# Kernel optimization log

Hardware: AMD Instinct MI355X
Metric: run time of the kernel (lower is better)

## Reference

```python
import jax, jax.numpy as jnp
import numpy as np
import math

BLUR_K = [1.0, 3.0, 3.0, 1.0]
EPS = 1e-8


def _make_blur_kernel(upsample_factor=2):
    k = jnp.asarray(BLUR_K, dtype=jnp.float32)
    k = k[None, :] * k[:, None]
    k = k / k.sum()
    return k * (upsample_factor ** 2)


def setup_inputs() -> dict:
    key = jax.random.key(0)
    ks = jax.random.split(key, 5)
    B, Cin, Cout, K, S, H, W = 16, 256, 128, 3, 512, 64, 64
    x = jax.random.normal(ks[0], (B, Cin, H, W), dtype=jnp.float32)
    style = jax.random.normal(ks[1], (B, S), dtype=jnp.float32)
    weight = jax.random.normal(ks[2], (1, Cout, Cin, K, K), dtype=jnp.float32)
    mod_w = jax.random.normal(ks[3], (Cin, S), dtype=jnp.float32) * (1.0 / math.sqrt(S))
    mod_b = jnp.ones((Cin,), dtype=jnp.float32)  # StyleGAN2 modulation bias init = 1
    return {"x": x, "style": style, "weight": weight, "mod_w": mod_w, "mod_b": mod_b}


def reference(x, style, weight, mod_w, mod_b):
    B, Cin, H, W = x.shape
    Cout = weight.shape[1]
    K = weight.shape[-1]
    scale = 1.0 / math.sqrt(Cin * K * K)

    # modulation: Linear(style_dim -> in_channel)
    s = style @ mod_w.T + mod_b                      # (B, Cin)
    w = scale * weight * s[:, None, :, None, None]   # (B, Cout, Cin, K, K)
    demod = jax.lax.rsqrt(jnp.sum(w * w, axis=(2, 3, 4)) + EPS)  # (B, Cout)
    w = w * demod[:, :, None, None, None]

    # per-sample conv_transpose2d(stride=2, padding=0, groups=B)
    # == lhs-dilated grouped correlation with spatially-flipped kernel
    kernel = jnp.flip(w, axis=(3, 4)).reshape(B * Cout, Cin, K, K)
    xg = x.reshape(1, B * Cin, H, W)
    out = jax.lax.conv_general_dilated(
        xg, kernel,
        window_strides=(1, 1),
        padding=((K - 1, K - 1), (K - 1, K - 1)),
        lhs_dilation=(2, 2),
        feature_group_count=B,
        dimension_numbers=("NCHW", "OIHW", "NCHW"),
    )  # (1, B*Cout, 2H+K-2, 2W+K-2) -> here (1, B*Cout, 2H+1, 2W+1)
    Ht, Wt = out.shape[2], out.shape[3]

    # Blur2 / upfirdn2d(up=1, down=1, pad=(pad0, pad1))
    # p = len(blur_kernel) - 2 - (K - 1); pad0 = (p+1)//2 + 1; pad1 = p//2 + 1
    p = len(BLUR_K) - 2 - (K - 1)
    pad0 = (p + 1) // 2 + 1
    pad1 = p // 2 + 1
    bk = _make_blur_kernel()                       # (4, 4)
    bw = jnp.flip(bk, axis=(0, 1))[None, None]     # (1, 1, 4, 4)
    outs = out.reshape(B * Cout, 1, Ht, Wt)
    blurred = jax.lax.conv_general_dilated(
        outs, bw,
        window_strides=(1, 1),
        padding=((pad0, pad1), (pad0, pad1)),
        dimension_numbers=("NCHW", "OIHW", "NCHW"),
    )
    Hb, Wb = blurred.shape[2], blurred.shape[3]
    return blurred.reshape(B, Cout, Hb, Wb)
```

## Files before the change

kernel.cpp:

```cpp
#include <hip/hip_runtime.h>
#include <stdint.h>

#define CIN 256
#define COUT 128
#define SDIM 512
#define NB 16

#define XP_RSTRIDE 16896
#define XP_BSTRIDE 1115136
#define A_BSTRIDE (512*2304)

typedef __attribute__((ext_vector_type(8))) short short8;
typedef __attribute__((ext_vector_type(4))) float f32x4;

__device__ __forceinline__ float bf2f(unsigned short h) {
  union { unsigned int u; float f; } v; v.u = ((unsigned int)h) << 16; return v.f;
}
__device__ __forceinline__ unsigned short f2bf(float f) {
  union { float f; unsigned int u; } v; v.f = f;
  return (unsigned short)((v.u + 0x7fffu + ((v.u >> 16) & 1u)) >> 16);
}
__device__ __forceinline__ void gll16(const void* g, void* l) {
  __builtin_amdgcn_global_load_lds(
      (const __attribute__((address_space(1))) unsigned int*)g,
      (__attribute__((address_space(3))) unsigned int*)l, 16, 0, 0);
}

__global__ __launch_bounds__(256) void k_detect(
    const unsigned short* __restrict__ xr, int* __restrict__ flag) {
  __shared__ int red[4];
  int t = threadIdx.x, cnt = 0;
  for (int i = t; i < 8192; i += 256) {
    int e = (xr[2*i] >> 7) & 0xff;
    cnt += (e > 90 && e < 145) ? 1 : 0;
  }
  #pragma unroll
  for (int off = 32; off > 0; off >>= 1) cnt += __shfl_down(cnt, off);
  if ((t & 63) == 0) red[t >> 6] = cnt;
  __syncthreads();
  if (t == 0) *flag = (red[0] + red[1] + red[2] + red[3] < 5000) ? 1 : 0;
}

__global__ __launch_bounds__(256) void k_style(
    const void* __restrict__ style_v, const void* __restrict__ mod_w_v,
    const void* __restrict__ mod_b_v, const int* __restrict__ flag,
    float* __restrict__ s_out) {
  __shared__ float st[SDIM];
  int b = blockIdx.x, t = threadIdx.x;
  int isf = *flag;
  float acc;
  if (!isf) {
    const unsigned short* style = (const unsigned short*)style_v;
    const unsigned short* mod_w = (const unsigned short*)mod_w_v;
    const unsigned short* mod_b = (const unsigned short*)mod_b_v;
    st[t]       = bf2f(style[b*SDIM + t]);
    st[t + 256] = bf2f(style[b*SDIM + t + 256]);
    __syncthreads();
    const uint4* wr = (const uint4*)(mod_w + (size_t)t*SDIM);
    acc = bf2f(mod_b[t]);
    #pragma unroll 4
    for (int s8 = 0; s8 < SDIM/8; ++s8) {
      uint4 p = wr[s8];
      int sb = s8*8;
      acc += bf2f((unsigned short)(p.x & 0xffff))*st[sb]
           + bf2f((unsigned short)(p.x >> 16))   *st[sb+1]
           + bf2f((unsigned short)(p.y & 0xffff))*st[sb+2]
           + bf2f((unsigned short)(p.y >> 16))   *st[sb+3]
           + bf2f((unsigned short)(p.z & 0xffff))*st[sb+4]
           + bf2f((unsigned short)(p.z >> 16))   *st[sb+5]
           + bf2f((unsigned short)(p.w & 0xffff))*st[sb+6]
           + bf2f((unsigned short)(p.w >> 16))   *st[sb+7];
    }
  } else {
    const float* style = (const float*)style_v;
    const float* mod_w = (const float*)mod_w_v;
    const float* mod_b = (const float*)mod_b_v;
    st[t]       = style[b*SDIM + t];
    st[t + 256] = style[b*SDIM + t + 256];
    __syncthreads();
    const float4* wr = (const float4*)(mod_w + (size_t)t*SDIM);
    acc = mod_b[t];
    #pragma unroll 4
    for (int s4 = 0; s4 < SDIM/4; ++s4) {
      float4 p = wr[s4];
      int sb = s4*4;
      acc += p.x*st[sb] + p.y*st[sb+1] + p.z*st[sb+2] + p.w*st[sb+3];
    }
  }
  s_out[b*CIN + t] = acc;
}

__global__ __launch_bounds__(256) void k_weights(
    const void* __restrict__ weight_v,
    const float* __restrict__ s_in,
    const int* __restrict__ flag,
    unsigned short* __restrict__ Aw) {
  int co = blockIdx.x, b = blockIdx.y, ci = threadIdx.x;
  int isf = *flag;
  float sm = 0.0208333333333333f * s_in[b*CIN + ci];
  float w9[9]; float ss = 0.f;
  if (!isf) {
    const unsigned short* wp = (const unsigned short*)weight_v + ((size_t)co*CIN + ci)*9;
    #pragma unroll
    for (int k = 0; k < 9; ++k) { float v = bf2f(wp[k]) * sm; w9[k] = v; ss += v*v; }
  } else {
    const float* wp = (const float*)weight_v + ((size_t)co*CIN + ci)*9;
    #pragma unroll
    for (int k = 0; k < 9; ++k) { float v = wp[k] * sm; w9[k] = v; ss += v*v; }
  }
  #pragma unroll
  for (int off = 32; off > 0; off >>= 1) ss += __shfl_down(ss, off);
  __shared__ float red[4];
  if ((ci & 63) == 0) red[ci >> 6] = ss;
  __syncthreads();
  float demod = rsqrtf(red[0] + red[1] + red[2] + red[3] + 1e-8f);
  #pragma unroll
  for (int k = 0; k < 9; ++k) w9[k] *= demod;
  const float F[4] = {0.25f, 0.75f, 0.75f, 0.25f};
  float C6[6][6];
  #pragma unroll
  for (int ty = 0; ty < 6; ++ty) {
    #pragma unroll
    for (int tx = 0; tx < 6; ++tx) {
      float acc = 0.f;
      #pragma unroll
      for (int ay = 0; ay < 3; ++ay) {
        int fy = ay - ty + 3;
        if (fy < 0 || fy > 3) continue;
        float ra = 0.f;
        #pragma unroll
        for (int ax = 0; ax < 3; ++ax) {
          int fx = ax - tx + 3;
          if (fx < 0 || fx > 3) continue;
          ra += w9[ay*3 + ax] * F[fx];
        }
        acc += ra * F[fy];
      }
      C6[ty][tx] = acc;
    }
  }
  unsigned short* Ab = Aw + (size_t)b*A_BSTRIDE;
  #pragma unroll
  for (int py = 0; py < 2; ++py) {
    #pragma unroll
    for (int px = 0; px < 2; ++px) {
      unsigned short* Am = Ab + (size_t)(py*256 + co*2 + px)*2304 + ci;
      #pragma unroll
      for (int dh = -1; dh <= 1; ++dh) {
        #pragma unroll
        for (int dw = -1; dw <= 1; ++dw) {
          int tap = (dh+1)*3 + (dw+1);
          Am[tap*256] = f2bf(C6[py - 2*dh + 2][px - 2*dw + 2]);
        }
      }
    }
  }
}

__global__ __launch_bounds__(256) void k_transpose(
    const void* __restrict__ x_v,
    const int* __restrict__ flag,
    unsigned short* __restrict__ xp) {
  int r_out = blockIdx.x, b = blockIdx.y, t = threadIdx.x;
  unsigned short* rp = xp + (size_t)b*XP_BSTRIDE + (size_t)r_out*XP_RSTRIDE;
  int r_in = r_out - 1;
  if (r_in < 0 || r_in >= 64) {
    uint4 z = make_uint4(0,0,0,0);
    #pragma unroll
    for (int i = 0; i < 9; ++i) {
      int idx = i*256 + t;
      if (idx < 2112) ((uint4*)rp)[idx] = z;
    }
    return;
  }
  if (t < 64) {
    uint4 z = make_uint4(0,0,0,0);
    int col = (t < 32) ? 0 : 65;
    ((uint4*)(rp + col*256))[t & 31] = z;
  }
  int isf = *flag;
  __shared__ unsigned int lds32[64*33];
  int tci = t >> 3;
  int tc8 = t & 7;
  int cS  = t >> 2;
  int jg  = t & 3;
  for (int g4 = 0; g4 < 4; ++g4) {
    int ci0 = g4 * 64;
    int ci = ci0 + tci*2;
    size_t base = (((size_t)b*CIN + ci)*64 + r_in)*64 + tc8*8;
    unsigned int v[8];
    if (isf) {
      const float* s0 = (const float*)x_v + base;
      const float* s1 = s0 + 4096;
      float4 a0 = ((const float4*)s0)[0], a1 = ((const float4*)s0)[1];
      float4 b0 = ((const float4*)s1)[0], b1 = ((const float4*)s1)[1];
      v[0] = f2bf(a0.x) | ((unsigned int)f2bf(b0.x) << 16);
      v[1] = f2bf(a0.y) | ((unsigned int)f2bf(b0.y) << 16);
      v[2] = f2bf(a0.z) | ((unsigned int)f2bf(b0.z) << 16);
      v[3] = f2bf(a0.w) | ((unsigned int)f2bf(b0.w) << 16);
      v[4] = f2bf(a1.x) | ((unsigned int)f2bf(b1.x) << 16);
      v[5] = f2bf(a1.y) | ((unsigned int)f2bf(b1.y) << 16);
      v[6] = f2bf(a1.z) | ((unsigned int)f2bf(b1.z) << 16);
      v[7] = f2bf(a1.w) | ((unsigned int)f2bf(b1.w) << 16);
    } else {
      const unsigned short* s0 = (const unsigned short*)x_v + base;
      const unsigned short* s1 = s0 + 4096;
      union { uint4 q; unsigned short h[8]; } u0, u1;
      u0.q = *(const uint4*)s0; u1.q = *(const uint4*)s1;
      #pragma unroll
      for (int j = 0; j < 8; ++j)
        v[j] = (unsigned int)u0.h[j] | ((unsigned int)u1.h[j] << 16);
    }
    if (g4) __syncthreads();
    #pragma unroll
    for (int j = 0; j < 8; ++j)
      lds32[(tc8*8 + j)*33 + tci] = v[j];
    __syncthreads();
    union { unsigned int o[8]; uint4 q[2]; } ob;
    #pragma unroll
    for (int w = 0; w < 8; ++w)
      ob.o[w] = lds32[cS*33 + jg*8 + w];
    uint4* dst = (uint4*)(rp + (size_t)(cS+1)*256 + ci0 + jg*16);
    dst[0] = ob.q[0];
    dst[1] = ob.q[1];
  }
}

__global__ __launch_bounds__(512, 2) void k_gemm(
    const unsigned short* __restrict__ Aw,
    const unsigned short* __restrict__ xp,
    const int* __restrict__ flag,
    void* __restrict__ out) {
  __shared__ __align__(16) unsigned short As[2][2][8192];
  __shared__ __align__(16) unsigned short Bs[2][2][8192];
  int g = blockIdx.x;
  int b  = ((g & 7) << 1) | ((g >> 3) & 1);
  int mt = (g >> 4) & 1;
  int nt = g >> 5;
  int yy0 = nt << 2;
  int t = threadIdx.x;
  int wave = t >> 6, lane = t & 63;
  int wm = wave >> 2, wn = wave & 3;
  int wh = wn >> 1, wr = wn & 1;
  int l15 = lane & 15, q = lane >> 4;
  int qs = q ^ ((l15 >> 2) & 3);
  int lOff = l15*32 + qs*8;
  int row = t >> 2, part = t & 3;
  int partS = part ^ ((row >> 2) & 3);
  int dst8 = t * 8;
  int isf = *flag;

  const unsigned short* pA0 = Aw + (size_t)b*A_BSTRIDE + (size_t)(mt*256 + row)*2304 + partS*8;
  const unsigned short* pA1 = pA0 + (size_t)128*2304;
  const unsigned short* pB0 = xp + (size_t)b*XP_BSTRIDE
      + (size_t)(yy0 + (row >> 6) + 1)*XP_RSTRIDE + (size_t)((row & 63) + 1)*256 + partS*8;
  const unsigned short* pB1 = pB0 + (size_t)2*XP_RSTRIDE;

  f32x4 acc[8][4];
  #pragma unroll
  for (int i = 0; i < 8; ++i)
    #pragma unroll
    for (int j = 0; j < 4; ++j)
      acc[i][j] = (f32x4){0.f, 0.f, 0.f, 0.f};

  #define BARR() do { asm volatile("" ::: "memory"); __builtin_amdgcn_s_barrier(); \
                      __builtin_amdgcn_sched_barrier(0); } while (0)
  #define LGKM0() do { asm volatile("s_waitcnt lgkmcnt(0)" ::: "memory"); \
                       __builtin_amdgcn_sched_barrier(0); } while (0)
  #define WVM8() do { asm volatile("s_waitcnt vmcnt(8)" ::: "memory"); \
                      __builtin_amdgcn_sched_barrier(0); } while (0)
  #define WVM4() do { asm volatile("s_waitcnt vmcnt(4)" ::: "memory"); \
                      __builtin_amdgcn_sched_barrier(0); } while (0)
  #define WVM0() do { asm volatile("s_waitcnt vmcnt(0)" ::: "memory"); \
                      __builtin_amdgcn_sched_barrier(0); } while (0)

  #define STG_A(D, H, KH, KT) gll16(pA##H + (KT)*64 + (KH)*32, &As[D][H][(KH)*4096 + dst8]);
  #define STG_B(D, H, KH, KT, DH, DW) \
    gll16(pB##H + (DH)*XP_RSTRIDE + (DW)*256 + ((KT)&3)*64 + (KH)*32, \
          &Bs[D][H][(KH)*4096 + dst8]);

  #define PH_READ_B(D, KH) { \
    _Pragma("unroll") \
    for (int j_ = 0; j_ < 4; ++j_) \
      bv[j_] = *(const short8*)&Bs[D][wh][(KH)*4096 + wr*2048 + j_*512 + lOff]; }
  #define PH_READ_A(D, KH, MQ) { \
    _Pragma("unroll") \
    for (int i_ = 0; i_ < 4; ++i_) \
      af[i_] = *(const short8*)&As[D][wm][(KH)*4096 + (MQ)*2048 + i_*512 + lOff]; }
  #define PH_MFMA(MQ) { \
    __builtin_amdgcn_s_setprio(1); \
    _Pragma("unroll") \
    for (int j_ = 0; j_ < 4; ++j_) \
      _Pragma("unroll") \
      for (int i_ = 0; i_ < 4; ++i_) \
        acc[(MQ)*4 + i_][j_] = __builtin_amdgcn_mfma_f32_16x16x32_bf16( \
            af[i_], bv[j_], acc[(MQ)*4 + i_][j_], 0, 0, 0); \
    __builtin_amdgcn_s_setprio(0); \
    __builtin_amdgcn_sched_barrier(0); }

  #define TILE(KT, D, E, DO1, DO0, WMID, WEND, DOEND) { \
    const int kt1_ = (KT) + 1, kt2_ = (KT) + 2; \
    int tap1_ = kt1_ >> 2; \
    int dh1_ = (tap1_ >= 6) ? 1 : ((tap1_ >= 3) ? 0 : -1); \
    int dw1_ = tap1_ - (dh1_ + 1)*3 - 1; \
    int tap2_ = kt2_ >> 2; \
    int dh2_ = (tap2_ >= 6) ? 1 : ((tap2_ >= 3) ? 0 : -1); \
    int dw2_ = tap2_ - (dh2_ + 1)*3 - 1; \
    short8 af[4], bv[4]; \
     \
    PH_READ_B(D, 0); PH_READ_A(D, 0, 0); \
    if (DO1) { STG_A(E, 0, 1, kt1_); STG_A(E, 1, 1, kt1_); } \
    BARR(); LGKM0(); PH_MFMA(0); BARR(); \
     \
    PH_READ_A(D, 0, 1); \
    if (DO1) { STG_B(E, 0, 1, kt1_, dh1_, dw1_); STG_B(E, 1, 1, kt1_, dh1_, dw1_); } \
    BARR(); LGKM0(); PH_MFMA(1); \
    WMID; BARR(); \
     \
    PH_READ_B(D, 1); PH_READ_A(D, 1, 0); \
    if (DO0) { STG_A(D, 0, 0, kt2_); STG_A(D, 1, 0, kt2_); } \
    BARR(); LGKM0(); PH_MFMA(0); BARR(); \
     \
    PH_READ_A(D, 1, 1); \
    if (DO0) { STG_B(D, 0, 0, kt2_, dh2_, dw2_); STG_B(D, 1, 0, kt2_, dh2_, dw2_); } \
    BARR(); LGKM0(); PH_MFMA(1); \
    if (DOEND) { WEND; BARR(); } \
  }

  STG_A(0, 0, 0, 0); STG_A(0, 1, 0, 0);
  STG_B(0, 0, 0, 0, -1, -1); STG_B(0, 1, 0, 0, -1, -1);
  STG_A(0, 0, 1, 0); STG_A(0, 1, 1, 0);
  STG_B(0, 0, 1, 0, -1, -1); STG_B(0, 1, 1, 0, -1, -1);
  STG_A(1, 0, 0, 1); STG_A(1, 1, 0, 1);
  STG_B(1, 0, 0, 1, -1, -1); STG_B(1, 1, 0, 1, -1, -1);
  WVM8(); BARR();

  #pragma unroll 1
  for (int kt = 0; kt < 34; kt += 2) {
    TILE(kt,     0, 1, 1, 1, WVM8(), WVM8(), 1);
    TILE(kt + 1, 1, 0, 1, 1, WVM8(), WVM8(), 1);
  }
  TILE(34, 0, 1, 1, 0, WVM8(), WVM4(), 1);
  TILE(35, 1, 0, 0, 0, WVM0(), WVM0(), 0);

  #undef TILE
  #undef PH_MFMA
  #undef PH_READ_A
  #undef PH_READ_B
  #undef STG_B
  #undef STG_A

  int y = 8*nt + 2*wn + mt;
  if (!isf) {
    unsigned int* outp = (unsigned int*)out;
    #pragma unroll
    for (int ig = 0; ig < 8; ++ig) {
      #pragma unroll
      for (int rr = 0; rr < 2; ++rr) {
        int co = wm*64 + (ig >> 2)*32 + (ig & 3)*8 + q*2 + rr;
        size_t obase = (((size_t)b*COUT + co)*128 + y)*64;
        #pragma unroll
        for (int j = 0; j < 4; ++j) {
          unsigned int pk = (unsigned int)f2bf(acc[ig][j][rr*2])
                          | ((unsigned int)f2bf(acc[ig][j][rr*2 + 1]) << 16);
          outp[obase + j*16 + l15] = pk;
        }
      }
    }
  } else {
    float2* outp = (float2*)out;
    #pragma unroll
    for (int ig = 0; ig < 8; ++ig) {
      #pragma unroll
      for (int rr = 0; rr < 2; ++rr) {
        int co = wm*64 + (ig >> 2)*32 + (ig & 3)*8 + q*2 + rr;
        size_t obase = (((size_t)b*COUT + co)*128 + y)*64;
        #pragma unroll
        for (int j = 0; j < 4; ++j)
          outp[obase + j*16 + l15] = make_float2(acc[ig][j][rr*2], acc[ig][j][rr*2 + 1]);
      }
    }
  }
  #undef BARR
  #undef LGKM0
  #undef WVM8
  #undef WVM4
  #undef WVM0
}

extern "C" void kernel_launch(void* const* d_in, const int* in_sizes, int n_in,
                              void* d_out, int out_size, void* d_ws, size_t ws_size,
                              hipStream_t stream) {
  const void* x      = d_in[0];
  const void* style  = d_in[1];
  const void* weight = d_in[2];
  const void* mod_w  = d_in[3];
  const void* mod_b  = d_in[4];
  char* ws = (char*)d_ws;
  int* flag           = (int*)ws;
  float* s_buf        = (float*)(ws + 1024);
  unsigned short* Aw  = (unsigned short*)(ws + 32768);
  unsigned short* xpd = (unsigned short*)(ws + 32768 + 37748736);

  k_detect   <<<1, 256, 0, stream>>>((const unsigned short*)x, flag);
  k_style    <<<NB, 256, 0, stream>>>(style, mod_w, mod_b, flag, s_buf);
  k_weights  <<<dim3(COUT, NB), 256, 0, stream>>>(weight, s_buf, flag, Aw);
  k_transpose<<<dim3(66, NB), 256, 0, stream>>>(x, flag, xpd);
  k_gemm     <<<512, 512, 0, stream>>>(Aw, xpd, flag, d_out);
}
```

Baseline: 386.5 us.

## Double-buffer LDS fragment registers to overlap ds_reads with MFMA in GEMM loop

Restructures the main GEMM tile loop so that LDS fragment reads for the next phase go into a second register set while MFMAs run on the current set. This removes the explicit lgkmcnt(0) waits and halves the barriers per phase. The vmcnt waits change from 8 to 6 to match the new ordering of global-to-LDS loads. The cost is higher VGPR pressure and more delicate correctness, since it now relies on compiler-inserted LDS waits and on the timing of barriers against async global_load_lds writes.

```diff
diff --git a/kernel.cpp b/kernel.cpp
--- a/kernel.cpp
+++ b/kernel.cpp
@@ -263,42 +263,50 @@
     for (int j = 0; j < 4; ++j)
       acc[i][j] = (f32x4){0.f, 0.f, 0.f, 0.f};
 
+  short8 afA0, afA1, afA2, afA3;
+  short8 afB0, afB1, afB2, afB3;
+  short8 bvA0, bvA1, bvA2, bvA3;
+  short8 bvB0, bvB1, bvB2, bvB3;
+
   #define BARR() do { asm volatile("" ::: "memory"); __builtin_amdgcn_s_barrier(); \
                       __builtin_amdgcn_sched_barrier(0); } while (0)
-  #define LGKM0() do { asm volatile("s_waitcnt lgkmcnt(0)" ::: "memory"); \
-                       __builtin_amdgcn_sched_barrier(0); } while (0)
-  #define WVM8() do { asm volatile("s_waitcnt vmcnt(8)" ::: "memory"); \
-                      __builtin_amdgcn_sched_barrier(0); } while (0)
-  #define WVM4() do { asm volatile("s_waitcnt vmcnt(4)" ::: "memory"); \
-                      __builtin_amdgcn_sched_barrier(0); } while (0)
-  #define WVM0() do { asm volatile("s_waitcnt vmcnt(0)" ::: "memory"); \
-                      __builtin_amdgcn_sched_barrier(0); } while (0)
+  #define SCHED0() __builtin_amdgcn_sched_barrier(0)
+  #define WVM8() do { asm volatile("s_waitcnt vmcnt(8)" ::: "memory"); } while (0)
+  #define WVM6() do { asm volatile("s_waitcnt vmcnt(6)" ::: "memory"); } while (0)
+  #define WVM4() do { asm volatile("s_waitcnt vmcnt(4)" ::: "memory"); } while (0)
+  #define WVM0() do { asm volatile("s_waitcnt vmcnt(0)" ::: "memory"); } while (0)
 
   #define STG_A(D, H, KH, KT) gll16(pA##H + (KT)*64 + (KH)*32, &As[D][H][(KH)*4096 + dst8]);
   #define STG_B(D, H, KH, KT, DH, DW) \
     gll16(pB##H + (DH)*XP_RSTRIDE + (DW)*256 + ((KT)&3)*64 + (KH)*32, \
           &Bs[D][H][(KH)*4096 + dst8]);
 
-  #define PH_READ_B(D, KH) { \
-    _Pragma("unroll") \
-    for (int j_ = 0; j_ < 4; ++j_) \
-      bv[j_] = *(const short8*)&Bs[D][wh][(KH)*4096 + wr*2048 + j_*512 + lOff]; }
-  #define PH_READ_A(D, KH, MQ) { \
-    _Pragma("unroll") \
-    for (int i_ = 0; i_ < 4; ++i_) \
-      af[i_] = *(const short8*)&As[D][wm][(KH)*4096 + (MQ)*2048 + i_*512 + lOff]; }
-  #define PH_MFMA(MQ) { \
+  #define RD_B(D, KH, V0, V1, V2, V3) { \
+    V0 = *(const short8*)&Bs[D][wh][(KH)*4096 + wr*2048 + 0*512 + lOff]; \
+    V1 = *(const short8*)&Bs[D][wh][(KH)*4096 + wr*2048 + 1*512 + lOff]; \
+    V2 = *(const short8*)&Bs[D][wh][(KH)*4096 + wr*2048 + 2*512 + lOff]; \
+    V3 = *(const short8*)&Bs[D][wh][(KH)*4096 + wr*2048 + 3*512 + lOff]; }
+  #define RD_A(D, KH, MQ, V0, V1, V2, V3) { \
+    V0 = *(const short8*)&As[D][wm][(KH)*4096 + (MQ)*2048 + 0*512 + lOff]; \
+    V1 = *(const short8*)&As[D][wm][(KH)*4096 + (MQ)*2048 + 1*512 + lOff]; \
+    V2 = *(const short8*)&As[D][wm][(KH)*4096 + (MQ)*2048 + 2*512 + lOff]; \
+    V3 = *(const short8*)&As[D][wm][(KH)*4096 + (MQ)*2048 + 3*512 + lOff]; }
+
+  #define MROW(AF, B0, B1, B2, B3, R) \
+    acc[R][0] = __builtin_amdgcn_mfma_f32_16x16x32_bf16(AF, B0, acc[R][0], 0, 0, 0); \
+    acc[R][1] = __builtin_amdgcn_mfma_f32_16x16x32_bf16(AF, B1, acc[R][1], 0, 0, 0); \
+    acc[R][2] = __builtin_amdgcn_mfma_f32_16x16x32_bf16(AF, B2, acc[R][2], 0, 0, 0); \
+    acc[R][3] = __builtin_amdgcn_mfma_f32_16x16x32_bf16(AF, B3, acc[R][3], 0, 0, 0);
+  #define MFMA16(A0, A1, A2, A3, B0, B1, B2, B3, MQ) { \
     __builtin_amdgcn_s_setprio(1); \
-    _Pragma("unroll") \
-    for (int j_ = 0; j_ < 4; ++j_) \
-      _Pragma("unroll") \
-      for (int i_ = 0; i_ < 4; ++i_) \
-        acc[(MQ)*4 + i_][j_] = __builtin_amdgcn_mfma_f32_16x16x32_bf16( \
-            af[i_], bv[j_], acc[(MQ)*4 + i_][j_], 0, 0, 0); \
+    MROW(A0, B0, B1, B2, B3, (MQ)*4 + 0) \
+    MROW(A1, B0, B1, B2, B3, (MQ)*4 + 1) \
+    MROW(A2, B0, B1, B2, B3, (MQ)*4 + 2) \
+    MROW(A3, B0, B1, B2, B3, (MQ)*4 + 3) \
     __builtin_amdgcn_s_setprio(0); \
-    __builtin_amdgcn_sched_barrier(0); }
-
-  #define TILE(KT, D, E, DO1, DO0, WMID, WEND, DOEND) { \
+    SCHED0(); }
+
+  #define TILE(KT, D, E, DO1, DO0, W1, W2, LAST) { \
     const int kt1_ = (KT) + 1, kt2_ = (KT) + 2; \
     int tap1_ = kt1_ >> 2; \
     int dh1_ = (tap1_ >= 6) ? 1 : ((tap1_ >= 3) ? 0 : -1); \
@@ -306,25 +314,34 @@
     int tap2_ = kt2_ >> 2; \
     int dh2_ = (tap2_ >= 6) ? 1 : ((tap2_ >= 3) ? 0 : -1); \
     int dw2_ = tap2_ - (dh2_ + 1)*3 - 1; \
-    short8 af[4], bv[4]; \
      \
-    PH_READ_B(D, 0); PH_READ_A(D, 0, 0); \
+    RD_A(D, 0, 1, afB0, afB1, afB2, afB3); \
     if (DO1) { STG_A(E, 0, 1, kt1_); STG_A(E, 1, 1, kt1_); } \
-    BARR(); LGKM0(); PH_MFMA(0); BARR(); \
+    SCHED0(); \
+    MFMA16(afA0, afA1, afA2, afA3, bvA0, bvA1, bvA2, bvA3, 0); \
      \
-    PH_READ_A(D, 0, 1); \
+    W1; BARR(); \
+    RD_B(D, 1, bvB0, bvB1, bvB2, bvB3); \
+    RD_A(D, 1, 0, afA0, afA1, afA2, afA3); \
     if (DO1) { STG_B(E, 0, 1, kt1_, dh1_, dw1_); STG_B(E, 1, 1, kt1_, dh1_, dw1_); } \
-    BARR(); LGKM0(); PH_MFMA(1); \
-    WMID; BARR(); \
+    SCHED0(); \
+    MFMA16(afB0, afB1, afB2, afB3, bvA0, bvA1, bvA2, bvA3, 1); \
+    BARR(); \
      \
-    PH_READ_B(D, 1); PH_READ_A(D, 1, 0); \
+    RD_A(D, 1, 1, afB0, afB1, afB2, afB3); \
     if (DO0) { STG_A(D, 0, 0, kt2_); STG_A(D, 1, 0, kt2_); } \
-    BARR(); LGKM0(); PH_MFMA(0); BARR(); \
+    SCHED0(); \
+    MFMA16(afA0, afA1, afA2, afA3, bvB0, bvB1, bvB2, bvB3, 0); \
      \
-    PH_READ_A(D, 1, 1); \
+    W2; BARR(); \
+    if (!(LAST)) { \
+      RD_B(E, 0, bvA0, bvA1, bvA2, bvA3); \
+      RD_A(E, 0, 0, afA0, afA1, afA2, afA3); \
+    } \
     if (DO0) { STG_B(D, 0, 0, kt2_, dh2_, dw2_); STG_B(D, 1, 0, kt2_, dh2_, dw2_); } \
-    BARR(); LGKM0(); PH_MFMA(1); \
-    if (DOEND) { WEND; BARR(); } \
+    SCHED0(); \
+    MFMA16(afB0, afB1, afB2, afB3, bvB0, bvB1, bvB2, bvB3, 1); \
+    BARR(); \
   }
 
   STG_A(0, 0, 0, 0); STG_A(0, 1, 0, 0);
@@ -334,19 +351,23 @@
   STG_A(1, 0, 0, 1); STG_A(1, 1, 0, 1);
   STG_B(1, 0, 0, 1, -1, -1); STG_B(1, 1, 0, 1, -1, -1);
   WVM8(); BARR();
+  RD_B(0, 0, bvA0, bvA1, bvA2, bvA3);
+  RD_A(0, 0, 0, afA0, afA1, afA2, afA3);
+  SCHED0();
 
   #pragma unroll 1
   for (int kt = 0; kt < 34; kt += 2) {
-    TILE(kt,     0, 1, 1, 1, WVM8(), WVM8(), 1);
-    TILE(kt + 1, 1, 0, 1, 1, WVM8(), WVM8(), 1);
-  }
-  TILE(34, 0, 1, 1, 0, WVM8(), WVM4(), 1);
-  TILE(35, 1, 0, 0, 0, WVM0(), WVM0(), 0);
+    TILE(kt,     0, 1, 1, 1, WVM6(), WVM6(), 0);
+    TILE(kt + 1, 1, 0, 1, 1, WVM6(), WVM6(), 0);
+  }
+  TILE(34, 0, 1, 1, 0, WVM6(), WVM4(), 0);
+  TILE(35, 1, 0, 0, 0, WVM0(), WVM0(), 1);
 
   #undef TILE
-  #undef PH_MFMA
-  #undef PH_READ_A
-  #undef PH_READ_B
+  #undef MFMA16
+  #undef MROW
+  #undef RD_A
+  #undef RD_B
   #undef STG_B
   #undef STG_A
 
@@ -382,8 +403,9 @@
     }
   }
   #undef BARR
-  #undef LGKM0
+  #undef SCHED0
   #undef WVM8
+  #undef WVM6
   #undef WVM4
   #undef WVM0
 }
```

Result: faster. 367.4 us (-4.9%).
